# Kernel tuning notes

Measured on AMD Instinct MI355X. Metric: run time of the kernel, lower is better.

The kernel has to match this reference:

```python
import jax, jax.numpy as jnp
import numpy as np

N_USERS = 100000
EMBED_DIM = 64
MAX_NEIGHBORS = 50
BATCH = 16384


def setup_inputs() -> dict:
    key = jax.random.key(0)
    k1, k2, k3, k4 = jax.random.split(key, 4)
    nodes = jax.random.randint(k1, (BATCH,), 0, N_USERS, dtype=jnp.int64 if jax.config.read('jax_enable_x64') else jnp.int32)
    u_u = jax.random.randint(k2, (N_USERS, MAX_NEIGHBORS), 0, N_USERS, dtype=nodes.dtype)
    # integer-valued degrees in [0, MAX_NEIGHBORS], zeros included to exercise the inf-mask
    u_u_l = jax.random.randint(k3, (N_USERS, 1), 0, MAX_NEIGHBORS + 1).astype(jnp.float32)
    emb = jax.random.normal(k4, (N_USERS, EMBED_DIM), dtype=jnp.float32)
    return {"nodes": nodes, "u_u": u_u, "u_u_l": u_u_l, "emb": emb}


def reference(nodes, u_u, u_u_l, emb):
    tem_adj = u_u[nodes]                    # [B, K] neighbor ids
    e_u = emb[tem_adj]                      # [B, K, D] gathered neighbor embeddings
    N_a = u_u_l[nodes]                      # [B, 1] degree of center node
    N_b = u_u_l[tem_adj][..., 0]            # [B, K] degree of neighbors
    att_w = 1.0 / (jnp.sqrt(N_a) * jnp.sqrt(N_b))  # [B, K]
    att_w = jnp.where(jnp.isinf(att_w), 0.0, att_w)
    # bmm(e_u^T [B,D,K], att_w [B,K,1]) -> [B,D]
    embed_matrix = jnp.einsum('bkd,bk->bd', e_u, att_w)
    return embed_matrix
```

## Files before the change

### kernel.cpp

```cpp
#include <hip/hip_runtime.h>

#define D 64
#define K 50
#define ROWS_PER_BLOCK 16
#define THREADS 256

__global__ __launch_bounds__(THREADS)
void social_agg_kernel(const int* __restrict__ nodes,
                       const int* __restrict__ u_u,
                       const float* __restrict__ u_u_l,
                       const float* __restrict__ emb,
                       float* __restrict__ out,
                       int batch)
{
    __shared__ uint2 nw[ROWS_PER_BLOCK][K];

    const int base = blockIdx.x * ROWS_PER_BLOCK;

    for (int p = threadIdx.x; p < ROWS_PER_BLOCK * K; p += THREADS) {
        const int r   = p / K;
        const int k   = p - r * K;
        const int row = base + r;
        int nb = 0; float w = 0.0f;
        if (row < batch) {
            const int   node = nodes[row];
            const float Na   = u_u_l[node];
            nb = u_u[node * K + k];
            const float Nb   = u_u_l[nb];
            const float prod = Na * Nb;
            w = (prod > 0.0f) ? rsqrtf(prod) : 0.0f;
        }
        nw[r][k] = make_uint2((unsigned)nb, __float_as_uint(w));
    }
    __syncthreads();

    const int lane = threadIdx.x & 63;
    const int wave = threadIdx.x >> 6;
    const int g    = lane >> 4;
    const int sub  = lane & 15;
    const int r    = wave * 4 + g;
    const int row  = base + r;

    float4 acc = make_float4(0.f, 0.f, 0.f, 0.f);
    #pragma unroll
    for (int k = 0; k < K; ++k) {
        const uint2  e  = nw[r][k];
        const float  wk = __uint_as_float(e.y);
        const float4 v  = *(const float4*)(emb + (size_t)e.x * D + sub * 4);
        acc.x += wk * v.x;
        acc.y += wk * v.y;
        acc.z += wk * v.z;
        acc.w += wk * v.w;
    }

    if (row < batch)
        *(float4*)(out + (size_t)row * D + sub * 4) = acc;
}

extern "C" void kernel_launch(void* const* d_in, const int* in_sizes, int n_in,
                              void* d_out, int out_size, void* d_ws, size_t ws_size,
                              hipStream_t stream) {
    const int*   nodes = (const int*)d_in[0];
    const int*   u_u   = (const int*)d_in[1];
    const float* u_u_l = (const float*)d_in[2];
    const float* emb   = (const float*)d_in[3];
    float*       out   = (float*)d_out;

    const int batch  = in_sizes[0];
    const int blocks = (batch + ROWS_PER_BLOCK - 1) / ROWS_PER_BLOCK;
    social_agg_kernel<<<blocks, THREADS, 0, stream>>>(
        nodes, u_u, u_u_l, emb, out, batch);
}
```

Measured before the change: 35.47 us.

## Split neighbor loop across lane groups with shuffle reduction, one row per wave

Each wave now handles one output row instead of four, with its four 16-lane groups splitting the 50 neighbors (padded to 52) and combining partial sums via xor shuffles. This shortens each thread's dependent gather chain from 50 to 13 iterations and quadruples the block count, aiming for more memory-level parallelism per row. In exchange it adds padding work, shuffle reduction overhead and four times as many blocks, each with a smaller prologue.

Result: faster. 34.20 us (-3.6%).

```diff
diff --git a/kernel.cpp b/kernel.cpp
--- a/kernel.cpp
+++ b/kernel.cpp
@@ -2,7 +2,9 @@
 
 #define D 64
 #define K 50
-#define ROWS_PER_BLOCK 16
+#define KK 4
+#define KPAD (KK * 13)
+#define ROWS_PER_BLOCK 4
 #define THREADS 256
 
 __global__ __launch_bounds__(THREADS)
@@ -13,38 +15,40 @@
                        float* __restrict__ out,
                        int batch)
 {
-    __shared__ uint2 nw[ROWS_PER_BLOCK][K];
+    __shared__ uint2 nw[ROWS_PER_BLOCK][KPAD];
 
     const int base = blockIdx.x * ROWS_PER_BLOCK;
 
-    for (int p = threadIdx.x; p < ROWS_PER_BLOCK * K; p += THREADS) {
-        const int r   = p / K;
-        const int k   = p - r * K;
-        const int row = base + r;
-        int nb = 0; float w = 0.0f;
-        if (row < batch) {
-            const int   node = nodes[row];
-            const float Na   = u_u_l[node];
-            nb = u_u[node * K + k];
-            const float Nb   = u_u_l[nb];
-            const float prod = Na * Nb;
-            w = (prod > 0.0f) ? rsqrtf(prod) : 0.0f;
+    {
+        const int p = threadIdx.x;
+        if (p < ROWS_PER_BLOCK * KPAD) {
+            const int r   = p / KPAD;
+            const int k   = p - r * KPAD;
+            const int row = base + r;
+            int nb = 0; float w = 0.0f;
+            if (row < batch && k < K) {
+                const int   node = nodes[row];
+                const float Na   = u_u_l[node];
+                nb = u_u[node * K + k];
+                const float Nb   = u_u_l[nb];
+                const float prod = Na * Nb;
+                w = (prod > 0.0f) ? rsqrtf(prod) : 0.0f;
+            }
+            nw[r][k] = make_uint2((unsigned)nb, __float_as_uint(w));
         }
-        nw[r][k] = make_uint2((unsigned)nb, __float_as_uint(w));
     }
     __syncthreads();
 
+    const int wave = threadIdx.x >> 6;
     const int lane = threadIdx.x & 63;
-    const int wave = threadIdx.x >> 6;
-    const int g    = lane >> 4;
+    const int kk   = lane >> 4;
     const int sub  = lane & 15;
-    const int r    = wave * 4 + g;
-    const int row  = base + r;
+    const int row  = base + wave;
 
     float4 acc = make_float4(0.f, 0.f, 0.f, 0.f);
     #pragma unroll
-    for (int k = 0; k < K; ++k) {
-        const uint2  e  = nw[r][k];
+    for (int i = 0; i < KPAD / KK; ++i) {
+        const uint2  e  = nw[wave][i * KK + kk];
         const float  wk = __uint_as_float(e.y);
         const float4 v  = *(const float4*)(emb + (size_t)e.x * D + sub * 4);
         acc.x += wk * v.x;
@@ -53,7 +57,15 @@
         acc.w += wk * v.w;
     }
 
-    if (row < batch)
+    #pragma unroll
+    for (int off = 16; off <= 32; off <<= 1) {
+        acc.x += __shfl_xor(acc.x, off);
+        acc.y += __shfl_xor(acc.y, off);
+        acc.z += __shfl_xor(acc.z, off);
+        acc.w += __shfl_xor(acc.w, off);
+    }
+
+    if (row < batch && kk == 0)
         *(float4*)(out + (size_t)row * D + sub * 4) = acc;
 }
 
```
